# Kernel tuning notes

Hardware: AMD Instinct MI355X
Metric: run time of the kernel (lower is better)

The kernel has to match this reference:

```python
import jax
import jax.numpy as jnp
from jax import lax
import numpy as np

EMBED_DIM = 768
NUM_HEADS = 12
BATCH = 8
SEQ = 1024
EPS = 1e-07
QK_QBIT = 8
QK_KBIT = 8
AV_ABIT = 8
AV_VBIT = 8
PROJ_WBIT = 8
PROJ_XBIT = 8
SCALE = EMBED_DIM ** (-0.5)  # module uses embed_dim, not head_dim


def _ste(hard, soft):
    # straight-through estimator: forward = hard, backward grad = d(soft)
    return soft + lax.stop_gradient(hard - soft)


def fake_quant_signed(x, bit):
    # _quantize_signed_matrix_train: sign/abs, global-max scaling, STE clamp + round
    sign = lax.stop_gradient(jnp.sign(x))
    a = jnp.abs(x)
    scaling = lax.stop_gradient(jnp.max(a)) + EPS
    y = a / scaling
    y = _ste(jnp.clip(y, 0.0, 1.0), y)          # Clamp.apply (STE)
    levels = 2.0 ** (bit - 1.0) - 1.0
    y = _ste(jnp.round(y * levels) / levels, y)  # Round.apply (STE)
    return y * scaling * sign


def fake_quant_unsigned(x, bit):
    # _quantize_unsigned_matrix_train
    scaling = lax.stop_gradient(jnp.max(x)) + EPS
    y = x / scaling
    y = _ste(jnp.clip(y, 0.0, 1.0), y)
    levels = 2.0 ** bit - 1.0
    y = _ste(jnp.round(y * levels) / levels, y)
    return y * scaling


def asim_linear(x, w, b, wbit, xbit):
    # ASiMLinear in 'Train' mode with signed_act=True: fake-quantize activation
    # and weight, dense matmul, trim_noise=0 -> no perturbation.
    xq = fake_quant_signed(x, xbit)
    wq = fake_quant_signed(w, wbit)
    return jnp.einsum('bnc,oc->bno', xq, wq) + b


def setup_inputs() -> dict:
    key = jax.random.key(0)
    k_x, k_qw, k_qb, k_pw, k_pb = jax.random.split(key, 5)
    x = jax.random.normal(k_x, (BATCH, SEQ, EMBED_DIM), dtype=jnp.float32)
    s = 1.0 / np.sqrt(EMBED_DIM)
    qkv_w = jax.random.normal(k_qw, (3 * EMBED_DIM, EMBED_DIM), dtype=jnp.float32) * s
    qkv_b = jax.random.normal(k_qb, (3 * EMBED_DIM,), dtype=jnp.float32) * 0.01
    proj_w = jax.random.normal(k_pw, (EMBED_DIM, EMBED_DIM), dtype=jnp.float32) * s
    proj_b = jax.random.normal(k_pb, (EMBED_DIM,), dtype=jnp.float32) * 0.01
    return {'x': x, 'qkv_w': qkv_w, 'qkv_b': qkv_b, 'proj_w': proj_w, 'proj_b': proj_b}


def reference(x, qkv_w, qkv_b, proj_w, proj_b):
    B, N, C = x.shape
    H = NUM_HEADS
    D = C // H
    # qkv projection (ASiMLinear, Train mode)
    qkv = asim_linear(x, qkv_w, qkv_b, PROJ_WBIT, PROJ_XBIT)      # [B, N, 3C]
    qkv = qkv.reshape(B, N, 3, H, D).transpose(2, 0, 3, 1, 4)      # [3, B, H, N, D]
    q, k, v = qkv[0], qkv[1], qkv[2]
    # _qk_train: fake-quantize q and k^T, matmul (trim_noise=0 -> no perturb)
    qq = fake_quant_signed(q, QK_QBIT)
    kq = fake_quant_signed(jnp.swapaxes(k, -2, -1), QK_KBIT)
    attn = jnp.einsum('bhnd,bhdm->bhnm', qq, kq) * SCALE           # [B, H, N, N]
    attn = jax.nn.softmax(attn, axis=-1)
    # dropout ratio 0.0 -> identity
    # _av_train: unsigned fake-quant of attention, signed fake-quant of v
    aq = fake_quant_unsigned(attn, AV_ABIT)
    vq = fake_quant_signed(v, AV_VBIT)
    out = jnp.einsum('bhnm,bhmd->bhnd', aq, vq)                    # [B, H, N, D]
    out = out.transpose(0, 2, 1, 3).reshape(B, N, C)
    # output projection (ASiMLinear, Train mode)
    out = asim_linear(out, proj_w, proj_b, PROJ_WBIT, PROJ_XBIT)
    return out
```

## Files before the change

### kernel.cpp

```cpp
#include <hip/hip_runtime.h>
#include <hip/hip_bf16.h>
#include <cstdint>
#include <cstddef>

#define B_    8
#define SEQ_  1024
#define C_    768
#define H_    12
#define D_    64
#define TC_   2304
#define M_    8192
#define EPS_  1e-7f
#define SCALE_ 0.036084391824351615f

typedef __attribute__((ext_vector_type(8))) short bf16x8;
typedef __attribute__((ext_vector_type(4))) float f32x4;

#define GLOAD_LDS16(gsrc, ldst) \
  __builtin_amdgcn_global_load_lds((const __attribute__((address_space(1))) unsigned int*)(gsrc), \
                                   (__attribute__((address_space(3))) unsigned int*)(ldst), 16, 0, 0)

__device__ __forceinline__ bf16x8 expand8(int2 raw) {
  union { int2 v; signed char c[8]; } u; u.v = raw;
  bf16x8 r;
  #pragma unroll
  for (int j = 0; j < 8; ++j) {
    float f = (float)(int)u.c[j];
    r[j] = (short)(__float_as_uint(f) >> 16);
  }
  return r;
}
__device__ __forceinline__ void expand16(int4 raw, int4& lo, int4& hi) {
  union { int4 v; signed char c[16]; } u; u.v = raw;
  unsigned short s[16];
  #pragma unroll
  for (int j = 0; j < 16; ++j) {
    float f = (float)(int)u.c[j];
    s[j] = (unsigned short)(__float_as_uint(f) >> 16);
  }
  lo = *(const int4*)&s[0]; hi = *(const int4*)&s[8];
}

__global__ void k_init(float* g) {
  if (threadIdx.x == 0) {
    g[0]=0.f; g[1]=0.f; g[2]=0.f; g[3]=0.f; g[4]=0.f; g[5]=0.f;
    g[6]=3.402823466e+38f;
    g[7]=0.f;
  }
}

__global__ __launch_bounds__(256) void k_absmax_fused(const float4* __restrict__ x,
                                                      const float4* __restrict__ w1,
                                                      const float4* __restrict__ w2,
                                                      float* g) {
  __shared__ float red[4];
  const int blk = blockIdx.x;
  const float4* p; unsigned n4; float* gout; int b0, nb;
  if (blk < 384)      { p = x;  n4 = 1572864u; gout = &g[0]; b0 = 0;   nb = 384; }
  else if (blk < 480) { p = w1; n4 = 442368u;  gout = &g[1]; b0 = 384; nb = 96;  }
  else                { p = w2; n4 = 147456u;  gout = &g[2]; b0 = 480; nb = 48;  }
  float m = 0.f;
  for (unsigned i = (unsigned)(blk - b0) * 256u + threadIdx.x; i < n4; i += (unsigned)nb * 256u) {
    float4 v = p[i];
    m = fmaxf(m, fmaxf(fmaxf(fabsf(v.x), fabsf(v.y)), fmaxf(fabsf(v.z), fabsf(v.w))));
  }
  #pragma unroll
  for (int off = 32; off; off >>= 1) m = fmaxf(m, __shfl_xor(m, off));
  if ((threadIdx.x & 63) == 0) red[threadIdx.x >> 6] = m;
  __syncthreads();
  if (threadIdx.x == 0) {
    m = fmaxf(fmaxf(red[0], red[1]), fmaxf(red[2], red[3]));
    atomicMax((unsigned int*)gout, __float_as_uint(m));
  }
}

__device__ __forceinline__ void quant_seg(const float* __restrict__ in, unsigned n, float s,
                                          unsigned short* __restrict__ out, unsigned i0, unsigned stride) {
  for (unsigned i = i0; i < n; i += stride) {
    float v = in[i];
    float y = fminf(fabsf(v) / s, 1.0f);
    float q = rintf(y * 127.0f);
    if (v < 0.f) q = -q;
    out[i] = (unsigned short)(__float_as_uint(q) >> 16);
  }
}
__global__ __launch_bounds__(256) void k_quant_fused(const float* __restrict__ x,
                                                     const float* __restrict__ w1,
                                                     const float* __restrict__ w2,
                                                     const float* __restrict__ g,
                                                     unsigned short* __restrict__ xq,
                                                     unsigned short* __restrict__ wq,
                                                     unsigned short* __restrict__ pw) {
  const int blk = blockIdx.x;
  if (blk < 1536)      quant_seg(x,  6291456u, g[0] + EPS_, xq, (unsigned)blk * 256u + threadIdx.x, 1536u * 256u);
  else if (blk < 1968) quant_seg(w1, 1769472u, g[1] + EPS_, wq, (unsigned)(blk - 1536) * 256u + threadIdx.x, 432u * 256u);
  else                 quant_seg(w2,  589824u, g[2] + EPS_, pw, (unsigned)(blk - 1968) * 256u + threadIdx.x, 144u * 256u);
}

__global__ __launch_bounds__(256) void k_quant_bf16(const float* __restrict__ in, unsigned n,
                                                    const float* __restrict__ gmax,
                                                    unsigned short* __restrict__ out) {
  const float s = *gmax + EPS_;
  quant_seg(in, n, s, out, blockIdx.x * blockDim.x + threadIdx.x, gridDim.x * blockDim.x);
}

__global__ __launch_bounds__(256) void k_gemm(const unsigned short* __restrict__ A,
                                              const unsigned short* __restrict__ Bt,
                                              const float* __restrict__ bias,
                                              float* __restrict__ C,
                                              int Mn, int Nn, int Kn,
                                              const float* __restrict__ sA, const float* __restrict__ sB,
                                              float* pmax, int partDiv) {
  __shared__ unsigned short As[2][128 * 64];
  __shared__ unsigned short Bs[2][128 * 64];
  const int tid = threadIdx.x;
  int flat = blockIdx.y * gridDim.x + blockIdx.x;
  int chunk = (gridDim.x * gridDim.y) >> 3;
  int nf = (flat & 7) * chunk + (flat >> 3);
  const int n0 = (nf % gridDim.x) * 128, m0 = (nf / gridDim.x) * 128;
  const int wid = tid >> 6, lane = tid & 63;
  const int wr = wid >> 1, wc = wid & 1;
  const int lrow = lane & 15;
  const int lko = (lane >> 4) << 3;
  f32x4 acc[4][4] = {};
  const int gr = (wid << 5) + (lane >> 3);
  const int gc = (((lane & 7) ^ ((lane >> 3) & 7)) << 3);
  const unsigned short* ga = A  + (size_t)(m0 + gr) * Kn + gc;
  const unsigned short* gb = Bt + (size_t)(n0 + gr) * Kn + gc;
  const int nt = Kn >> 6;
  #pragma unroll
  for (int c = 0; c < 4; ++c) {
    GLOAD_LDS16(ga + (size_t)(c * 8) * Kn, &As[0][(wid * 32 + c * 8) * 64]);
    GLOAD_LDS16(gb + (size_t)(c * 8) * Kn, &Bs[0][(wid * 32 + c * 8) * 64]);
  }
  asm volatile("s_waitcnt vmcnt(0)" ::: "memory");
  __syncthreads();
  int cur = 0;
  for (int t = 0; t < nt; ++t) {
    if (t + 1 < nt) {
      #pragma unroll
      for (int c = 0; c < 4; ++c) {
        GLOAD_LDS16(ga + (size_t)(c * 8) * Kn + (t + 1) * 64, &As[cur ^ 1][(wid * 32 + c * 8) * 64]);
        GLOAD_LDS16(gb + (size_t)(c * 8) * Kn + (t + 1) * 64, &Bs[cur ^ 1][(wid * 32 + c * 8) * 64]);
      }
    }
    const char* Ab = (const char*)As[cur];
    const char* Bb = (const char*)Bs[cur];
    #pragma unroll
    for (int kk = 0; kk < 64; kk += 32) {
      bf16x8 af[4], bfr[4];
      #pragma unroll
      for (int i = 0; i < 4; ++i) {
        int row = wr * 64 + i * 16 + lrow;
        af[i] = *(const bf16x8*)(Ab + ((row * 128 + (kk + lko) * 2) ^ ((row & 7) << 4)));
      }
      #pragma unroll
      for (int j = 0; j < 4; ++j) {
        int row = wc * 64 + j * 16 + lrow;
        bfr[j] = *(const bf16x8*)(Bb + ((row * 128 + (kk + lko) * 2) ^ ((row & 7) << 4)));
      }
      #pragma unroll
      for (int i = 0; i < 4; ++i)
        #pragma unroll
        for (int j = 0; j < 4; ++j)
          acc[i][j] = __builtin_amdgcn_mfma_f32_16x16x32_bf16(af[i], bfr[j], acc[i][j], 0, 0, 0);
    }
    asm volatile("s_waitcnt vmcnt(0)" ::: "memory");
    __syncthreads();
    cur ^= 1;
  }
  const float alpha = (sA[0] + EPS_) * (sB[0] + EPS_) * (1.0f / 16129.0f);
  const int orow = (lane >> 4) << 2;
  float amax = 0.f;
  #pragma unroll
  for (int i = 0; i < 4; ++i) {
    #pragma unroll
    for (int j = 0; j < 4; ++j) {
      int col = n0 + wc * 64 + j * 16 + lrow;
      float bc = bias[col];
      #pragma unroll
      for (int rr = 0; rr < 4; ++rr) {
        int row = m0 + wr * 64 + i * 16 + orow + rr;
        float val = acc[i][j][rr] * alpha + bc;
        C[(size_t)row * Nn + col] = val;
        amax = fmaxf(amax, fabsf(val));
      }
    }
  }
  if (pmax) {
    #pragma unroll
    for (int off = 32; off; off >>= 1) amax = fmaxf(amax, __shfl_xor(amax, off));
    if (lane == 0) atomicMax((unsigned int*)&pmax[n0 / partDiv], __float_as_uint(amax));
  }
}

__global__ __launch_bounds__(256) void k_quant_heads(const float* __restrict__ qkvf, const float* __restrict__ g,
                                                     int8_t* __restrict__ qo, int8_t* __restrict__ ko,
                                                     int8_t* __restrict__ vT) {
  const unsigned total = (unsigned)M_ * TC_;
  const float s0 = g[3] + EPS_, s1 = g[4] + EPS_, s2 = g[5] + EPS_;
  for (unsigned i = blockIdx.x * blockDim.x + threadIdx.x; i < total; i += gridDim.x * blockDim.x) {
    unsigned m = i / 2304u, o = i % 2304u;
    unsigned part = o / 768u, c = o % 768u;
    unsigned h = c >> 6, d = c & 63;
    unsigned b = m >> 10, n = m & 1023;
    float s = (part == 0) ? s0 : (part == 1) ? s1 : s2;
    float v = qkvf[i];
    float y = fminf(fabsf(v) / s, 1.0f);
    int q = (int)rintf(y * 127.0f);
    if (v < 0.f) q = -q;
    unsigned bh = b * 12 + h;
    if (part == 0)      qo[((size_t)bh * 1024 + n) * 64 + d] = (int8_t)q;
    else if (part == 1) ko[((size_t)bh * 1024 + n) * 64 + d] = (int8_t)q;
    else                vT[((size_t)bh * 64 + d) * 1024 + n] = (int8_t)q;
  }
}

__global__ __launch_bounds__(256) void k_attn_stats_mfma(
    const int8_t* __restrict__ qi8, const int8_t* __restrict__ ki8,
    const float* __restrict__ g, float* __restrict__ rowmax, float* __restrict__ denomv,
    unsigned int* __restrict__ gminden) {
  __shared__ unsigned short Ks[64 * 64];
  __shared__ float red[4];
  const int bh = blockIdx.x >> 4, rt = blockIdx.x & 15;
  const int tid = threadIdx.x, w = tid >> 6, lane = tid & 63;
  const int lrow = lane & 15, lko = (lane >> 4) << 3;
  const int8_t* qbase = qi8 + (size_t)bh * 65536;
  const int8_t* kbase = ki8 + (size_t)bh * 65536;
  bf16x8 qf[2];
  #pragma unroll
  for (int ks = 0; ks < 2; ++ks)
    qf[ks] = expand8(*(const int2*)(qbase + (size_t)(rt*64 + w*16 + lrow) * 64 + ks*32 + lko));
  const float qkScale = (g[3] + EPS_) * (g[4] + EPS_) * (1.0f / 16129.0f) * SCALE_;
  float m = -3.0e38f, den = 0.f;
  const int srow = tid >> 2, sc = tid & 3;
  const int sx = (srow & 7) << 4;
  int4 kraw = *(const int4*)(kbase + (size_t)srow * 64 + sc * 16);
  for (int t = 0; t < 16; ++t) {
    __syncthreads();
    {
      int4 lo, hi; expand16(kraw, lo, hi);
      int bb = srow * 128 + sc * 32;
      *(int4*)((char*)Ks + ( bb       ^ sx)) = lo;
      *(int4*)((char*)Ks + ((bb + 16) ^ sx)) = hi;
    }
    if (t < 15)
      kraw = *(const int4*)(kbase + (size_t)(t + 1) * 4096 + (size_t)srow * 64 + sc * 16);
    __syncthreads();
    f32x4 acc[4] = {};
    #pragma unroll
    for (int ks = 0; ks < 2; ++ks)
      #pragma unroll
      for (int j = 0; j < 4; ++j) {
        int row = j * 16 + lrow;
        bf16x8 kf = *(const bf16x8*)((const char*)Ks + ((row * 128 + (ks*32 + lko) * 2) ^ ((row & 7) << 4)));
        acc[j] = __builtin_amdgcn_mfma_f32_16x16x32_bf16(kf, qf[ks], acc[j], 0, 0, 0);
      }
    float mnew = m;
    #pragma unroll
    for (int j = 0; j < 4; ++j)
      #pragma unroll
      for (int rr = 0; rr < 4; ++rr)
        mnew = fmaxf(mnew, acc[j][rr] * qkScale);
    float d = den * __expf(m - mnew);
    #pragma unroll
    for (int j = 0; j < 4; ++j)
      #pragma unroll
      for (int rr = 0; rr < 4; ++rr)
        d += __expf(acc[j][rr] * qkScale - mnew);
    den = d; m = mnew;
  }
  #pragma unroll
  for (int off = 16; off <= 32; off <<= 1) {
    float mo = __shfl_xor(m, off);
    float doo = __shfl_xor(den, off);
    float mg = fmaxf(m, mo);
    den = den * __expf(m - mg) + doo * __expf(mo - mg);
    m = mg;
  }
  if (lane < 16) {
    size_t rg = (size_t)bh * 1024 + rt * 64 + w * 16 + lane;
    rowmax[rg] = m;
    denomv[rg] = den;
  }
  float bm = den;
  #pragma unroll
  for (int off = 1; off < 16; off <<= 1) bm = fminf(bm, __shfl_xor(bm, off));
  if (lane == 0) red[w] = bm;
  __syncthreads();
  if (tid == 0)
    atomicMin(gminden, __float_as_uint(fminf(fminf(red[0], red[1]), fminf(red[2], red[3]))));
}

__global__ __launch_bounds__(256) void k_attn_pv_mfma(
    const int8_t* __restrict__ qi8, const int8_t* __restrict__ ki8, const int8_t* __restrict__ vti8,
    const float* __restrict__ g, const unsigned int* __restrict__ gminden,
    const float* __restrict__ rowmax, const float* __restrict__ denomv,
    float* __restrict__ aof, float* __restrict__ gamax) {
  __shared__ unsigned short Ks[64 * 64];
  __shared__ unsigned short Vs[64 * 64];
  __shared__ unsigned short Ps[64 * 64];
  __shared__ float red[4];
  const int bh = blockIdx.x >> 4, rt = blockIdx.x & 15;
  const int b = bh / 12, h = bh % 12;
  const int tid = threadIdx.x, w = tid >> 6, lane = tid & 63;
  const int lrow = lane & 15, lko = (lane >> 4) << 3;
  const int8_t* qbase = qi8 + (size_t)bh * 65536;
  const int8_t* kbase = ki8 + (size_t)bh * 65536;
  const int8_t* vbase = vti8 + (size_t)bh * 65536;
  bf16x8 qf[2];
  #pragma unroll
  for (int ks = 0; ks < 2; ++ks)
    qf[ks] = expand8(*(const int2*)(qbase + (size_t)(rt*64 + w*16 + lrow) * 64 + ks*32 + lko));
  const float qkScale = (g[3] + EPS_) * (g[4] + EPS_) * (1.0f / 16129.0f) * SCALE_;
  const float minden = __uint_as_float(*gminden);
  const float sa = 1.0f / minden + EPS_;
  const float invSa = 1.0f / sa;
  const float sv = g[5] + EPS_;
  const float pvScale = sa * sv * (1.0f / 32385.0f);
  const float rm  = rowmax[(size_t)bh * 1024 + rt * 64 + w * 16 + lrow];
  const float ivd = 1.0f / denomv[(size_t)bh * 1024 + rt * 64 + w * 16 + lrow];
  f32x4 accO[4] = {};
  const int srow = tid >> 2, sc = tid & 3;
  const int sx = (srow & 7) << 4;
  int4 kraw = *(const int4*)(kbase + (size_t)srow * 64 + sc * 16);
  int4 vraw = *(const int4*)(vbase + (size_t)srow * 1024 + sc * 16);
  for (int t = 0; t < 16; ++t) {
    __syncthreads();
    {
      int4 lo, hi;
      int bb = srow * 128 + sc * 32;
      expand16(kraw, lo, hi);
      *(int4*)((char*)Ks + ( bb       ^ sx)) = lo;
      *(int4*)((char*)Ks + ((bb + 16) ^ sx)) = hi;
      expand16(vraw, lo, hi);
      *(int4*)((char*)Vs + ( bb       ^ sx)) = lo;
      *(int4*)((char*)Vs + ((bb + 16) ^ sx)) = hi;
    }
    if (t < 15) {
      kraw = *(const int4*)(kbase + (size_t)(t + 1) * 4096 + (size_t)srow * 64 + sc * 16);
      vraw = *(const int4*)(vbase + (size_t)srow * 1024 + (t + 1) * 64 + sc * 16);
    }
    __syncthreads();
    f32x4 acc[4] = {};
    #pragma unroll
    for (int ks = 0; ks < 2; ++ks)
      #pragma unroll
      for (int j = 0; j < 4; ++j) {
        int row = j * 16 + lrow;
        bf16x8 kf = *(const bf16x8*)((const char*)Ks + ((row * 128 + (ks*32 + lko) * 2) ^ ((row & 7) << 4)));
        acc[j] = __builtin_amdgcn_mfma_f32_16x16x32_bf16(kf, qf[ks], acc[j], 0, 0, 0);
      }
    const int q = w * 16 + lrow;
    const int kb = (lane >> 4) << 2;
    #pragma unroll
    for (int j = 0; j < 4; ++j) {
      float a0 = rintf(fminf(__expf(acc[j][0] * qkScale - rm) * ivd * invSa, 1.0f) * 255.0f);
      float a1 = rintf(fminf(__expf(acc[j][1] * qkScale - rm) * ivd * invSa, 1.0f) * 255.0f);
      float a2 = rintf(fminf(__expf(acc[j][2] * qkScale - rm) * ivd * invSa, 1.0f) * 255.0f);
      float a3 = rintf(fminf(__expf(acc[j][3] * qkScale - rm) * ivd * invSa, 1.0f) * 255.0f);
      uint2 pk;
      pk.x = (__float_as_uint(a0) >> 16) | ((__float_as_uint(a1) >> 16) << 16);
      pk.y = (__float_as_uint(a2) >> 16) | ((__float_as_uint(a3) >> 16) << 16);
      int byteoff = (q * 128 + (j * 16 + kb) * 2) ^ ((q & 7) << 4);
      *(uint2*)((char*)Ps + byteoff) = pk;
    }
    #pragma unroll
    for (int ks = 0; ks < 2; ++ks) {
      bf16x8 pf = *(const bf16x8*)((const char*)Ps + ((q * 128 + (ks*32 + lko) * 2) ^ ((q & 7) << 4)));
      #pragma unroll
      for (int j = 0; j < 4; ++j) {
        int row = j * 16 + lrow;
        bf16x8 vf = *(const bf16x8*)((const char*)Vs + ((row * 128 + (ks*32 + lko) * 2) ^ ((row & 7) << 4)));
        accO[j] = __builtin_amdgcn_mfma_f32_16x16x32_bf16(pf, vf, accO[j], 0, 0, 0);
      }
    }
  }
  float amax = 0.f;
  #pragma unroll
  for (int j = 0; j < 4; ++j) {
    int d = j * 16 + lrow;
    #pragma unroll
    for (int rr = 0; rr < 4; ++rr) {
      int row = rt * 64 + w * 16 + (lane >> 4) * 4 + rr;
      float val = accO[j][rr] * pvScale;
      aof[((size_t)(b * 1024 + row)) * 768 + h * 64 + d] = val;
      amax = fmaxf(amax, fabsf(val));
    }
  }
  #pragma unroll
  for (int off = 1; off < 64; off <<= 1) amax = fmaxf(amax, __shfl_xor(amax, off));
  if (lane == 0) red[w] = amax;
  __syncthreads();
  if (tid == 0)
    atomicMax((unsigned int*)gamax, __float_as_uint(fmaxf(fmaxf(red[0], red[1]), fmaxf(red[2], red[3]))));
}

extern "C" void kernel_launch(void* const* d_in, const int* in_sizes, int n_in,
                              void* d_out, int out_size, void* d_ws, size_t ws_size,
                              hipStream_t stream) {
  const float* x      = (const float*)d_in[0];
  const float* qkv_w  = (const float*)d_in[1];
  const float* qkv_b  = (const float*)d_in[2];
  const float* proj_w = (const float*)d_in[3];
  const float* proj_b = (const float*)d_in[4];
  float* out = (float*)d_out;

  char* w = (char*)d_ws;
  float*          g      = (float*)(w + 0);
  float*          rowmax = (float*)(w + 256);
  float*          denomv = (float*)(w + 393472);
  int8_t*         qi8    = (int8_t*)(w + 786688);
  int8_t*         ki8    = (int8_t*)(w + 7078144);
  int8_t*         vT     = (int8_t*)(w + 13369600);
  unsigned short* pw     = (unsigned short*)(w + 19661056);
  unsigned short* xq     = (unsigned short*)(w + 20840704);
  unsigned short* wq     = (unsigned short*)(w + 33423616);
  float*          qkvf   = (float*)(w + 36962560);
  float*          aof    = (float*)(w + 36962560);
  unsigned short* aobf   = (unsigned short*)(w + 62128384);

  hipLaunchKernelGGL(k_init, dim3(1), dim3(64), 0, stream, g);

  hipLaunchKernelGGL(k_absmax_fused, dim3(528), dim3(256), 0, stream,
                     (const float4*)x, (const float4*)qkv_w, (const float4*)proj_w, g);

  hipLaunchKernelGGL(k_quant_fused, dim3(2112), dim3(256), 0, stream,
                     x, qkv_w, proj_w, g, xq, wq, pw);

  hipLaunchKernelGGL(k_gemm, dim3(TC_ / 128, M_ / 128), dim3(256), 0, stream,
                     xq, wq, qkv_b, qkvf, M_, TC_, C_, &g[0], &g[1], &g[3], 768);

  hipLaunchKernelGGL(k_quant_heads, dim3(2048), dim3(256), 0, stream, qkvf, g, qi8, ki8, vT);

  hipLaunchKernelGGL(k_attn_stats_mfma, dim3(1536), dim3(256), 0, stream,
                     qi8, ki8, g, rowmax, denomv, (unsigned int*)&g[6]);
  hipLaunchKernelGGL(k_attn_pv_mfma, dim3(1536), dim3(256), 0, stream,
                     qi8, ki8, vT, g, (const unsigned int*)&g[6], rowmax, denomv, aof, &g[7]);

  hipLaunchKernelGGL(k_quant_bf16, dim3(2048), dim3(256), 0, stream, aof, 6291456u, &g[7], aobf);

  hipLaunchKernelGGL(k_gemm, dim3(C_ / 128, M_ / 128), dim3(256), 0, stream,
                     aobf, pw, proj_b, out, M_, C_, C_, &g[7], &g[2], (float*)nullptr, 1);

  (void)in_sizes; (void)n_in; (void)out_size; (void)ws_size;
}
```

Measured before the change: 277.1 us.

## Store quantized GEMM operands as int8 and expand to bf16 in LDS

The quantize kernels now write int8 instead of bf16 for the activations, weights and attention output. The projection GEMMs load these int8 tiles into registers, widen them to bf16, and store them swizzled into a single LDS buffer. This halves global traffic for the quantized operands. In exchange, the async global-to-LDS double buffering is replaced by register prefetch plus per-tile expansion ALU work and an extra barrier.

```diff
diff --git a/kernel.cpp b/kernel.cpp
--- a/kernel.cpp
+++ b/kernel.cpp
@@ -15,10 +15,6 @@
 
 typedef __attribute__((ext_vector_type(8))) short bf16x8;
 typedef __attribute__((ext_vector_type(4))) float f32x4;
-
-#define GLOAD_LDS16(gsrc, ldst) \
-  __builtin_amdgcn_global_load_lds((const __attribute__((address_space(1))) unsigned int*)(gsrc), \
-                                   (__attribute__((address_space(3))) unsigned int*)(ldst), 16, 0, 0)
 
 __device__ __forceinline__ bf16x8 expand8(int2 raw) {
   union { int2 v; signed char c[8]; } u; u.v = raw;
@@ -74,45 +70,45 @@
   }
 }
 
-__device__ __forceinline__ void quant_seg(const float* __restrict__ in, unsigned n, float s,
-                                          unsigned short* __restrict__ out, unsigned i0, unsigned stride) {
+__device__ __forceinline__ void quant_seg8(const float* __restrict__ in, unsigned n, float s,
+                                           int8_t* __restrict__ out, unsigned i0, unsigned stride) {
   for (unsigned i = i0; i < n; i += stride) {
     float v = in[i];
     float y = fminf(fabsf(v) / s, 1.0f);
-    float q = rintf(y * 127.0f);
+    int q = (int)rintf(y * 127.0f);
     if (v < 0.f) q = -q;
-    out[i] = (unsigned short)(__float_as_uint(q) >> 16);
+    out[i] = (int8_t)q;
   }
 }
 __global__ __launch_bounds__(256) void k_quant_fused(const float* __restrict__ x,
                                                      const float* __restrict__ w1,
                                                      const float* __restrict__ w2,
                                                      const float* __restrict__ g,
-                                                     unsigned short* __restrict__ xq,
-                                                     unsigned short* __restrict__ wq,
-                                                     unsigned short* __restrict__ pw) {
+                                                     int8_t* __restrict__ xq,
+                                                     int8_t* __restrict__ wq,
+                                                     int8_t* __restrict__ pw) {
   const int blk = blockIdx.x;
-  if (blk < 1536)      quant_seg(x,  6291456u, g[0] + EPS_, xq, (unsigned)blk * 256u + threadIdx.x, 1536u * 256u);
-  else if (blk < 1968) quant_seg(w1, 1769472u, g[1] + EPS_, wq, (unsigned)(blk - 1536) * 256u + threadIdx.x, 432u * 256u);
-  else                 quant_seg(w2,  589824u, g[2] + EPS_, pw, (unsigned)(blk - 1968) * 256u + threadIdx.x, 144u * 256u);
-}
-
-__global__ __launch_bounds__(256) void k_quant_bf16(const float* __restrict__ in, unsigned n,
-                                                    const float* __restrict__ gmax,
-                                                    unsigned short* __restrict__ out) {
+  if (blk < 1536)      quant_seg8(x,  6291456u, g[0] + EPS_, xq, (unsigned)blk * 256u + threadIdx.x, 1536u * 256u);
+  else if (blk < 1968) quant_seg8(w1, 1769472u, g[1] + EPS_, wq, (unsigned)(blk - 1536) * 256u + threadIdx.x, 432u * 256u);
+  else                 quant_seg8(w2,  589824u, g[2] + EPS_, pw, (unsigned)(blk - 1968) * 256u + threadIdx.x, 144u * 256u);
+}
+
+__global__ __launch_bounds__(256) void k_quant_i8(const float* __restrict__ in, unsigned n,
+                                                  const float* __restrict__ gmax,
+                                                  int8_t* __restrict__ out) {
   const float s = *gmax + EPS_;
-  quant_seg(in, n, s, out, blockIdx.x * blockDim.x + threadIdx.x, gridDim.x * blockDim.x);
-}
-
-__global__ __launch_bounds__(256) void k_gemm(const unsigned short* __restrict__ A,
-                                              const unsigned short* __restrict__ Bt,
-                                              const float* __restrict__ bias,
-                                              float* __restrict__ C,
-                                              int Mn, int Nn, int Kn,
-                                              const float* __restrict__ sA, const float* __restrict__ sB,
-                                              float* pmax, int partDiv) {
-  __shared__ unsigned short As[2][128 * 64];
-  __shared__ unsigned short Bs[2][128 * 64];
+  quant_seg8(in, n, s, out, blockIdx.x * blockDim.x + threadIdx.x, gridDim.x * blockDim.x);
+}
+
+__global__ __launch_bounds__(256) void k_gemm8(const int8_t* __restrict__ A,
+                                               const int8_t* __restrict__ Bt,
+                                               const float* __restrict__ bias,
+                                               float* __restrict__ C,
+                                               int Mn, int Nn, int Kn,
+                                               const float* __restrict__ sA, const float* __restrict__ sB,
+                                               float* pmax, int partDiv) {
+  __shared__ unsigned short As[128 * 64];
+  __shared__ unsigned short Bs[128 * 64];
   const int tid = threadIdx.x;
   int flat = blockIdx.y * gridDim.x + blockIdx.x;
   int chunk = (gridDim.x * gridDim.y) >> 3;
@@ -123,41 +119,55 @@
   const int lrow = lane & 15;
   const int lko = (lane >> 4) << 3;
   f32x4 acc[4][4] = {};
-  const int gr = (wid << 5) + (lane >> 3);
-  const int gc = (((lane & 7) ^ ((lane >> 3) & 7)) << 3);
-  const unsigned short* ga = A  + (size_t)(m0 + gr) * Kn + gc;
-  const unsigned short* gb = Bt + (size_t)(n0 + gr) * Kn + gc;
+  const int r0 = tid >> 2;
+  const int c0 = tid & 3;
+  const int8_t* ga = A  + (size_t)m0 * Kn;
+  const int8_t* gb = Bt + (size_t)n0 * Kn;
   const int nt = Kn >> 6;
-  #pragma unroll
-  for (int c = 0; c < 4; ++c) {
-    GLOAD_LDS16(ga + (size_t)(c * 8) * Kn, &As[0][(wid * 32 + c * 8) * 64]);
-    GLOAD_LDS16(gb + (size_t)(c * 8) * Kn, &Bs[0][(wid * 32 + c * 8) * 64]);
-  }
-  asm volatile("s_waitcnt vmcnt(0)" ::: "memory");
-  __syncthreads();
-  int cur = 0;
+  int4 ra0 = *(const int4*)(ga + (size_t)r0 * Kn + c0 * 16);
+  int4 ra1 = *(const int4*)(ga + (size_t)(64 + r0) * Kn + c0 * 16);
+  int4 rb0 = *(const int4*)(gb + (size_t)r0 * Kn + c0 * 16);
+  int4 rb1 = *(const int4*)(gb + (size_t)(64 + r0) * Kn + c0 * 16);
   for (int t = 0; t < nt; ++t) {
+    if (t) __syncthreads();
+    {
+      int4 lo, hi;
+      const int sx0 = (r0 & 7) << 4;
+      const int bb0 = r0 * 128 + c0 * 32;
+      const int bb1 = (64 + r0) * 128 + c0 * 32;
+      expand16(ra0, lo, hi);
+      *(int4*)((char*)As + ( bb0       ^ sx0)) = lo;
+      *(int4*)((char*)As + ((bb0 + 16) ^ sx0)) = hi;
+      expand16(ra1, lo, hi);
+      *(int4*)((char*)As + ( bb1       ^ sx0)) = lo;
+      *(int4*)((char*)As + ((bb1 + 16) ^ sx0)) = hi;
+      expand16(rb0, lo, hi);
+      *(int4*)((char*)Bs + ( bb0       ^ sx0)) = lo;
+      *(int4*)((char*)Bs + ((bb0 + 16) ^ sx0)) = hi;
+      expand16(rb1, lo, hi);
+      *(int4*)((char*)Bs + ( bb1       ^ sx0)) = lo;
+      *(int4*)((char*)Bs + ((bb1 + 16) ^ sx0)) = hi;
+    }
     if (t + 1 < nt) {
-      #pragma unroll
-      for (int c = 0; c < 4; ++c) {
-        GLOAD_LDS16(ga + (size_t)(c * 8) * Kn + (t + 1) * 64, &As[cur ^ 1][(wid * 32 + c * 8) * 64]);
-        GLOAD_LDS16(gb + (size_t)(c * 8) * Kn + (t + 1) * 64, &Bs[cur ^ 1][(wid * 32 + c * 8) * 64]);
-      }
-    }
-    const char* Ab = (const char*)As[cur];
-    const char* Bb = (const char*)Bs[cur];
+      const int ko = (t + 1) * 64;
+      ra0 = *(const int4*)(ga + (size_t)r0 * Kn + ko + c0 * 16);
+      ra1 = *(const int4*)(ga + (size_t)(64 + r0) * Kn + ko + c0 * 16);
+      rb0 = *(const int4*)(gb + (size_t)r0 * Kn + ko + c0 * 16);
+      rb1 = *(const int4*)(gb + (size_t)(64 + r0) * Kn + ko + c0 * 16);
+    }
+    __syncthreads();
     #pragma unroll
     for (int kk = 0; kk < 64; kk += 32) {
       bf16x8 af[4], bfr[4];
       #pragma unroll
       for (int i = 0; i < 4; ++i) {
         int row = wr * 64 + i * 16 + lrow;
-        af[i] = *(const bf16x8*)(Ab + ((row * 128 + (kk + lko) * 2) ^ ((row & 7) << 4)));
+        af[i] = *(const bf16x8*)((const char*)As + ((row * 128 + (kk + lko) * 2) ^ ((row & 7) << 4)));
       }
       #pragma unroll
       for (int j = 0; j < 4; ++j) {
         int row = wc * 64 + j * 16 + lrow;
-        bfr[j] = *(const bf16x8*)(Bb + ((row * 128 + (kk + lko) * 2) ^ ((row & 7) << 4)));
+        bfr[j] = *(const bf16x8*)((const char*)Bs + ((row * 128 + (kk + lko) * 2) ^ ((row & 7) << 4)));
       }
       #pragma unroll
       for (int i = 0; i < 4; ++i)
@@ -165,9 +175,6 @@
         for (int j = 0; j < 4; ++j)
           acc[i][j] = __builtin_amdgcn_mfma_f32_16x16x32_bf16(af[i], bfr[j], acc[i][j], 0, 0, 0);
     }
-    asm volatile("s_waitcnt vmcnt(0)" ::: "memory");
-    __syncthreads();
-    cur ^= 1;
   }
   const float alpha = (sA[0] + EPS_) * (sB[0] + EPS_) * (1.0f / 16129.0f);
   const int orow = (lane >> 4) << 2;
@@ -413,12 +420,12 @@
   int8_t*         qi8    = (int8_t*)(w + 786688);
   int8_t*         ki8    = (int8_t*)(w + 7078144);
   int8_t*         vT     = (int8_t*)(w + 13369600);
-  unsigned short* pw     = (unsigned short*)(w + 19661056);
-  unsigned short* xq     = (unsigned short*)(w + 20840704);
-  unsigned short* wq     = (unsigned short*)(w + 33423616);
+  int8_t*         pw8    = (int8_t*)(w + 19661056);
+  int8_t*         xq8    = (int8_t*)(w + 20840704);
+  int8_t*         wq8    = (int8_t*)(w + 33423616);
   float*          qkvf   = (float*)(w + 36962560);
   float*          aof    = (float*)(w + 36962560);
-  unsigned short* aobf   = (unsigned short*)(w + 62128384);
+  int8_t*         aob8   = (int8_t*)(w + 62128384);
 
   hipLaunchKernelGGL(k_init, dim3(1), dim3(64), 0, stream, g);
 
@@ -426,10 +433,10 @@
                      (const float4*)x, (const float4*)qkv_w, (const float4*)proj_w, g);
 
   hipLaunchKernelGGL(k_quant_fused, dim3(2112), dim3(256), 0, stream,
-                     x, qkv_w, proj_w, g, xq, wq, pw);
-
-  hipLaunchKernelGGL(k_gemm, dim3(TC_ / 128, M_ / 128), dim3(256), 0, stream,
-                     xq, wq, qkv_b, qkvf, M_, TC_, C_, &g[0], &g[1], &g[3], 768);
+                     x, qkv_w, proj_w, g, xq8, wq8, pw8);
+
+  hipLaunchKernelGGL(k_gemm8, dim3(TC_ / 128, M_ / 128), dim3(256), 0, stream,
+                     xq8, wq8, qkv_b, qkvf, M_, TC_, C_, &g[0], &g[1], &g[3], 768);
 
   hipLaunchKernelGGL(k_quant_heads, dim3(2048), dim3(256), 0, stream, qkvf, g, qi8, ki8, vT);
 
@@ -438,10 +445,10 @@
   hipLaunchKernelGGL(k_attn_pv_mfma, dim3(1536), dim3(256), 0, stream,
                      qi8, ki8, vT, g, (const unsigned int*)&g[6], rowmax, denomv, aof, &g[7]);
 
-  hipLaunchKernelGGL(k_quant_bf16, dim3(2048), dim3(256), 0, stream, aof, 6291456u, &g[7], aobf);
-
-  hipLaunchKernelGGL(k_gemm, dim3(C_ / 128, M_ / 128), dim3(256), 0, stream,
-                     aobf, pw, proj_b, out, M_, C_, C_, &g[7], &g[2], (float*)nullptr, 1);
+  hipLaunchKernelGGL(k_quant_i8, dim3(2048), dim3(256), 0, stream, aof, 6291456u, &g[7], aob8);
+
+  hipLaunchKernelGGL(k_gemm8, dim3(C_ / 128, M_ / 128), dim3(256), 0, stream,
+                     aob8, pw8, proj_b, out, M_, C_, C_, &g[7], &g[2], (float*)nullptr, 1);
 
   (void)in_sizes; (void)n_in; (void)out_size; (void)ws_size;
 }
```

Result: faster. 269.4 us (-2.8%).
